# Kernel tuning notes

Hardware: AMD Instinct MI355X
Metric: run time of the kernel (lower is better)

Reference implementation:

```python
import jax, jax.numpy as jnp
import numpy as np

B, K, R, H = 64, 256, 4, 32


def setup_inputs() -> dict:
    key = jax.random.key(0)
    ks = jax.random.split(key, 24)
    rn = lambda k, s: jax.random.normal(k, s, dtype=jnp.float32)
    # F.normalize(dim=0) on per-sample [n, R] factors -> normalize columns (axis=1 batched)
    norm_cols = lambda x: x / jnp.linalg.norm(x, axis=1, keepdims=True)
    I = jnp.eye(K, dtype=jnp.float32)
    return dict(
        tensor_input=rn(ks[0], (B, 6, K, K)),
        seed_ic=rn(ks[1], (B, K)),
        seed_sir=rn(ks[2], (B, K)),
        seed_ic_conv=rn(ks[3], (B, K)),
        seed_sir_conv=rn(ks[4], (B, K)),
        scalars=rn(ks[5], (B, 2)),
        second_eig_interlink_out=rn(ks[6], (B,)),
        second_eig_interlink_in=rn(ks[7], (B,)),
        S1=I + 0.1 * rn(ks[8], (K, K)),
        S2=I + 0.1 * rn(ks[9], (K, K)),
        S3=I + 0.1 * rn(ks[10], (K, K)),
        S4=I + 0.1 * rn(ks[11], (K, K)),
        # CP factors (fresh random per sample in torch; fixed here for determinism)
        cp_A=norm_cols(rn(ks[12], (B, 6, R))),
        cp_B=norm_cols(rn(ks[13], (B, K, R))),
        cp_C=norm_cols(rn(ks[14], (B, K, R))),
        cp_W1=0.1 * rn(ks[15], (R, H, 3)), cp_b1=jnp.zeros((R, H), jnp.float32),
        cp_w2=0.1 * rn(ks[16], (R, H)), cp_b2=jnp.zeros((R,), jnp.float32),
        seed_W1=0.1 * rn(ks[17], (4, H, K)), seed_b1=jnp.zeros((4, H), jnp.float32),
        seed_w2=0.1 * rn(ks[18], (4, H)), seed_b2=jnp.zeros((4,), jnp.float32),
        fin_W1=0.1 * rn(ks[19], (H, R + 6)), fin_b1=jnp.zeros((H,), jnp.float32),
        fin_w2=0.1 * rn(ks[20], (H,)), fin_b2=jnp.zeros((), jnp.float32),
    )


def reference(tensor_input, seed_ic, seed_sir, seed_ic_conv, seed_sir_conv, scalars,
              second_eig_interlink_out, second_eig_interlink_in,
              S1, S2, S3, S4, cp_A, cp_B, cp_C,
              cp_W1, cp_b1, cp_w2, cp_b2,
              seed_W1, seed_b1, seed_w2, seed_b2,
              fin_W1, fin_b1, fin_w2, fin_b2):
    Kd = S1.shape[0]
    I = jnp.eye(Kd, dtype=tensor_input.dtype)
    ic1, ic2, sir1, sir2 = tensor_input[:, 0], tensor_input[:, 1], tensor_input[:, 2], tensor_input[:, 3]
    Z1r, Z2r = tensor_input[:, 4], tensor_input[:, 5]

    # MatrixTransform chains == plain batched matmuls (custom backward = standard matmul vjp)
    Z1 = ((ic1 @ S1) @ Z1r @ S2) @ jnp.swapaxes(sir2, -1, -2)   # [B,K,K]
    Z2 = ((sir1 @ S3) @ Z2r @ S4) @ jnp.swapaxes(ic2, -1, -2)   # [B,K,K]

    def spec_loss(val, M):
        ev = jnp.linalg.eigvalsh(M)                 # ascending, lower-triangle (matches torch)
        eig_loss = jnp.mean(jnp.abs(val - ev[1:5])) # k = min(5, K) = 5
        diff = jnp.mean(jnp.abs(M - I))             # reg_loss and diff_from_identity are identical
        off_loss = -jnp.mean(jnp.abs(M - jnp.diag(jnp.diag(M))))
        loss = eig_loss + 0.1 * diff + 0.1 * diff + 0.1 * off_loss
        return jnp.where(val != 0.0, loss, jnp.zeros_like(loss))  # torch: `if value`

    spec_out = jax.vmap(spec_loss)(second_eig_interlink_out, Z1).mean()
    spec_in = jax.vmap(spec_loss)(second_eig_interlink_in, Z2).mean()

    # S-matrix regularizers (batch-independent) + per-sample transform loss.
    # The torch list interleaves them, so the mean = 0.5*s_total + 0.5*mean(transform).
    sreg = lambda S: -jnp.mean(jnp.abs(S - I)) - jnp.mean(jnp.abs(S - jnp.diag(jnp.diag(S))))
    s_total = sreg(S1) + sreg(S2) + sreg(S3) + sreg(S4)
    transform = jnp.mean(jnp.abs(Z1 - Z1r), axis=(1, 2)) + jnp.mean(jnp.abs(Z2 - Z2r), axis=(1, 2))
    s_matrix_mean = 0.5 * s_total + 0.5 * transform.mean()

    # CP reconstruction loss on tensor with slots 4,5 replaced by Z1,Z2
    T_upd = jnp.concatenate([tensor_input[:, :4], Z1[:, None], Z2[:, None]], axis=1)  # [B,6,K,K]
    recon = jnp.einsum('bir,bjr,bkr->bijk', cp_A, cp_B, cp_C)
    cp_loss = jnp.mean((recon - T_upd) ** 2)

    # Per-rank tiny MLPs on factor means
    triple = jnp.stack([cp_A.mean(axis=1), cp_B.mean(axis=1), cp_C.mean(axis=1)], axis=-1)  # [B,R,3]
    h = jax.nn.relu(jnp.einsum('brd,rhd->brh', triple, cp_W1) + cp_b1[None])
    cp_s = jnp.einsum('brh,rh->br', h, cp_w2) + cp_b2[None]                                 # [B,R]

    seeds = jnp.stack([seed_ic, seed_sir, seed_ic_conv, seed_sir_conv], axis=1)             # [B,4,K]
    h2 = jax.nn.relu(jnp.einsum('bjk,jhk->bjh', seeds, seed_W1) + seed_b1[None])
    seed_s = jnp.einsum('bjh,jh->bj', h2, seed_w2) + seed_b2[None]                          # [B,4]

    combined = jnp.concatenate([cp_s, seed_s, scalars], axis=1)                             # [B,R+6]
    logits = jax.nn.relu(combined @ fin_W1.T + fin_b1) @ fin_w2 + fin_b2                    # [B]

    return (logits, spec_out, spec_in, cp_loss, s_matrix_mean)
```

## Files before the change

kernel.cpp:

```cpp
#include <hip/hip_runtime.h>
#include <hip/hip_fp16.h>

#define LM 24

#define OFF_MP    0ull
#define OFF_Q0    16777216ull
#define OFF_Q1    33554432ull
#define OFF_ZB    33554432ull
#define OFF_EIG   50331648ull
#define OFF_DIFFP (OFF_EIG + 4096ull)
#define OFF_OFFP  (OFF_DIFFP + 1024ull)
#define OFF_TRP   (OFF_OFFP + 1024ull)
#define OFF_SMALL (OFF_TRP + 1024ull)

typedef unsigned short ushort_t;
typedef short bf16x8 __attribute__((ext_vector_type(8)));
typedef float f32x4 __attribute__((ext_vector_type(4)));

static __device__ __forceinline__ ushort_t f2bf(float f) {
  unsigned u = __float_as_uint(f);
  unsigned r = (u + 0x7fffu + ((u >> 16) & 1u)) >> 16;
  return (ushort_t)r;
}
static __device__ __forceinline__ unsigned packbf(float a, float b) {
  return (unsigned)f2bf(a) | ((unsigned)f2bf(b) << 16);
}
static __device__ __forceinline__ float bflo(unsigned u) { return __uint_as_float(u << 16); }
static __device__ __forceinline__ float bfhi(unsigned u) { return __uint_as_float(u & 0xffff0000u); }
static __device__ __forceinline__ float b2f(ushort_t u) { return __uint_as_float(((unsigned)u) << 16); }
static __device__ __forceinline__ __half2 u2h2(unsigned u) { __half2 r; *reinterpret_cast<unsigned*>(&r) = u; return r; }
static __device__ __forceinline__ unsigned packh2(float a, float b) {
  return (unsigned)__half_as_ushort(__float2half_rn(a)) |
         ((unsigned)__half_as_ushort(__float2half_rn(b)) << 16);
}

template<bool ABF, int BMODE, bool INITP, bool REDUCE>
__global__ __launch_bounds__(256) void gemm_mfma(
    const void* __restrict__ A0, const void* __restrict__ A1, size_t sA,
    const void* __restrict__ B0, const void* __restrict__ B1, size_t sB,
    void* __restrict__ Cbase, size_t sC,
    const float* __restrict__ Zr0, const float* __restrict__ Zr1, size_t sZr,
    double* __restrict__ smallp, double* __restrict__ diffP,
    double* __restrict__ offP, double* __restrict__ trP)
{
  __shared__ ushort_t At[128][40];
  __shared__ ushort_t Bt[128][40];
  __shared__ float redsh[4][3];
  const int t = threadIdx.x;
  if (INITP && blockIdx.x == 0 && blockIdx.y == 0 && blockIdx.z == 0) {
    if (t < 2) smallp[t] = 0.0;
    if (t < 128) { diffP[t] = 0.0; offP[t] = 0.0; trP[t] = 0.0; }
  }
  const int b = blockIdx.z;
  const int bl = (b < 64) ? b : b - 64;
  const void* Ab_ = (b < 64) ? A0 : A1;
  const void* Bb_ = (b < 64) ? B0 : B1;
  const int tm = blockIdx.y * 128, tn = blockIdx.x * 128;
  const int w = t >> 6, l = t & 63;
  const int wr = w >> 1, wc = w & 1;
  const int fr = l & 15, kc = l >> 4;

  f32x4 acc[4][4] = {};

  for (int s8 = 0; s8 < 8; ++s8) {
    const int k0 = s8 << 5;
    #pragma unroll
    for (int cc = 0; cc < 2; ++cc) {
      int c = t + cc * 256;
      int row = c >> 2, q = c & 3;
      if (ABF) {
        const ushort_t* Ap = (const ushort_t*)Ab_ + (size_t)bl * sA + (size_t)(tm + row) * 256 + k0 + q * 8;
        *(uint4*)&At[row][q * 8] = *(const uint4*)Ap;
      } else {
        const float* Ap = (const float*)Ab_ + (size_t)bl * sA + (size_t)(tm + row) * 256 + k0 + q * 8;
        float4 f0 = *(const float4*)Ap, f1 = *(const float4*)(Ap + 4);
        uint4 u;
        u.x = packbf(f0.x, f0.y); u.y = packbf(f0.z, f0.w);
        u.z = packbf(f1.x, f1.y); u.w = packbf(f1.z, f1.w);
        *(uint4*)&At[row][q * 8] = u;
      }
    }
    if (BMODE == 1) {
      #pragma unroll
      for (int cc = 0; cc < 2; ++cc) {
        int c = t + cc * 256;
        int row = c >> 2, q = c & 3;
        const float* Bp = (const float*)Bb_ + (size_t)bl * sB + (size_t)(tn + row) * 256 + k0 + q * 8;
        float4 f0 = *(const float4*)Bp, f1 = *(const float4*)(Bp + 4);
        uint4 u;
        u.x = packbf(f0.x, f0.y); u.y = packbf(f0.z, f0.w);
        u.z = packbf(f1.x, f1.y); u.w = packbf(f1.z, f1.w);
        *(uint4*)&Bt[row][q * 8] = u;
      }
    } else {
      int k2 = t & 15, c = t >> 4;
      const float* Bp0 = (const float*)Bb_ + (size_t)bl * sB + (size_t)(k0 + 2 * k2) * 256 + tn + c * 8;
      const float* Bp1 = Bp0 + 256;
      float4 a0 = *(const float4*)Bp0, a1 = *(const float4*)(Bp0 + 4);
      float4 c0v = *(const float4*)Bp1, c1v = *(const float4*)(Bp1 + 4);
      float lo[8] = {a0.x,a0.y,a0.z,a0.w,a1.x,a1.y,a1.z,a1.w};
      float hi[8] = {c0v.x,c0v.y,c0v.z,c0v.w,c1v.x,c1v.y,c1v.z,c1v.w};
      unsigned* Bd = (unsigned*)&Bt[0][0];
      #pragma unroll
      for (int i = 0; i < 8; ++i) {
        int n = c * 8 + i;
        Bd[n * 20 + k2] = packbf(lo[i], hi[i]);
      }
    }
    __syncthreads();
    bf16x8 af[4], bfv[4];
    #pragma unroll
    for (int i = 0; i < 4; ++i) af[i] = *(const bf16x8*)&At[wr * 64 + i * 16 + fr][kc * 8];
    #pragma unroll
    for (int jj = 0; jj < 4; ++jj) bfv[jj] = *(const bf16x8*)&Bt[wc * 64 + jj * 16 + fr][kc * 8];
    #pragma unroll
    for (int i = 0; i < 4; ++i) {
      #pragma unroll
      for (int jj = 0; jj < 4; ++jj) {
        acc[i][jj] = __builtin_amdgcn_mfma_f32_16x16x32_bf16(af[i], bfv[jj], acc[i][jj], 0, 0, 0);
      }
    }
    __syncthreads();
  }

  ushort_t* Cp = (ushort_t*)Cbase + (size_t)b * sC;
  #pragma unroll
  for (int i = 0; i < 4; ++i) {
    #pragma unroll
    for (int q = 0; q < 4; ++q) {
      size_t rbase = (size_t)(tm + wr * 64 + i * 16 + kc * 4 + q) * 256;
      #pragma unroll
      for (int jj = 0; jj < 4; ++jj) {
        Cp[rbase + tn + wc * 64 + jj * 16 + fr] = f2bf(acc[i][jj][q]);
      }
    }
  }

  if (REDUCE) {
    const float* Zr_ = ((b < 64) ? Zr0 : Zr1) + (size_t)bl * sZr;
    float pd = 0.f, po = 0.f, ptr = 0.f;
    #pragma unroll
    for (int i = 0; i < 4; ++i) {
      #pragma unroll
      for (int q = 0; q < 4; ++q) {
        int row = tm + wr * 64 + i * 16 + kc * 4 + q;
        const float* ZrRow = Zr_ + (size_t)row * 256 + tn + wc * 64;
        #pragma unroll
        for (int jj = 0; jj < 4; ++jj) {
          int col = tn + wc * 64 + jj * 16 + fr;
          float c = acc[i][jj][q];
          float zr = ZrRow[jj * 16 + fr];
          bool diag = (row == col);
          pd += fabsf(c - (diag ? 1.0f : 0.0f));
          po += diag ? 0.0f : fabsf(c);
          ptr += fabsf(c - zr);
        }
      }
    }
    #pragma unroll
    for (int off = 32; off > 0; off >>= 1) {
      pd += __shfl_down(pd, off);
      po += __shfl_down(po, off);
      ptr += __shfl_down(ptr, off);
    }
    if (l == 0) { redsh[w][0] = pd; redsh[w][1] = po; redsh[w][2] = ptr; }
    __syncthreads();
    if (t == 0) {
      atomicAdd(&diffP[b], (double)(redsh[0][0] + redsh[1][0] + redsh[2][0] + redsh[3][0]));
      atomicAdd(&offP[b],  (double)(redsh[0][1] + redsh[1][1] + redsh[2][1] + redsh[3][1]));
      atomicAdd(&trP[b],   (double)(redsh[0][2] + redsh[1][2] + redsh[2][2] + redsh[3][2]));
    }
  }
}

__global__ __launch_bounds__(256) void symm_t(const ushort_t* __restrict__ Zb,
                                              unsigned* __restrict__ Mp)
{
  __shared__ unsigned Au[64][38];
  __shared__ unsigned Bu[64][38];
  const int blk = blockIdx.x;
  const int mtx = blk / 10, p = blk - mtx * 10;
  const int bi_t[10] = {0,0,0,0,1,1,1,2,2,3};
  const int bj_t[10] = {0,1,2,3,1,2,3,2,3,3};
  const int bi = bi_t[p], bj = bj_t[p];
  const ushort_t* Z = Zb + (size_t)mtx * 65536;
  const int t = threadIdx.x;
  #pragma unroll
  for (int it = 0; it < 4; ++it) {
    int idx = t + it * 256;
    int row = idx >> 4, jj = idx & 15;
    uint2 va = *(const uint2*)(Z + (size_t)(bi * 64 + row) * 256 + bj * 64 + jj * 4);
    uint2 vb = *(const uint2*)(Z + (size_t)(bj * 64 + row) * 256 + bi * 64 + jj * 4);
    Au[row][jj * 2] = va.x; Au[row][jj * 2 + 1] = va.y;
    Bu[row][jj * 2] = vb.x; Bu[row][jj * 2 + 1] = vb.y;
  }
  __syncthreads();
  const float SC = 0.5f * 0.015625f;
  const int r = t & 63, kbase = (t >> 6) * 8;
  unsigned* MpM = Mp + (size_t)mtx * 32768;
  const bool odd = (r & 1);
  #pragma unroll
  for (int i = 0; i < 8; ++i) {
    int k = kbase + i;
    unsigned a = Au[r][k];
    unsigned bu0 = Bu[2 * k][r >> 1], bu1 = Bu[2 * k + 1][r >> 1];
    float b0 = odd ? bfhi(bu0) : bflo(bu0);
    float b1 = odd ? bfhi(bu1) : bflo(bu1);
    MpM[(size_t)(bj * 32 + k) * 256 + bi * 64 + r] =
        packh2((bflo(a) + b0) * SC, (bfhi(a) + b1) * SC);
  }
  if (bi != bj) {
    #pragma unroll
    for (int i = 0; i < 8; ++i) {
      int k = kbase + i;
      unsigned a = Bu[r][k];
      unsigned au0 = Au[2 * k][r >> 1], au1 = Au[2 * k + 1][r >> 1];
      float a0 = odd ? bfhi(au0) : bflo(au0);
      float a1 = odd ? bfhi(au1) : bflo(au1);
      MpM[(size_t)(bi * 32 + k) * 256 + bj * 64 + r] =
          packh2((bflo(a) + a0) * SC, (bfhi(a) + a1) * SC);
    }
  }
}

struct LanSh {
  unsigned vpack[128];
  float wtmp[4][256];
  float red2[4][2];
  float red1[16];
  float alpha[LM];
  float betaArr[LM + 1];
  float beta2arr[LM + 1];
};
struct CpSh { float Bsh[4][256][4]; float Csh[4][256][4]; double red[4][256]; };
struct SregSh { double red[4][256]; };
struct HeadSh {
  float Wl[32][258];
  float seedsl[8][256];
  float hbuf2[8][128];
  float tri[8][4][3];
  float cps[8][4];
  float seds[8][4];
};
union MegaSh { LanSh lan; CpSh cp; SregSh sreg; HeadSh head; };

__global__ __launch_bounds__(1024, 1) void mega_kernel(
    const unsigned* __restrict__ Mp, float* __restrict__ eig,
    const float* __restrict__ ti, const ushort_t* __restrict__ Zb,
    const float* __restrict__ cpA, const float* __restrict__ cpB, const float* __restrict__ cpC,
    double* __restrict__ smallp,
    const float* __restrict__ S1, const float* __restrict__ S2,
    const float* __restrict__ S3, const float* __restrict__ S4,
    const float* __restrict__ seed_ic, const float* __restrict__ seed_sir,
    const float* __restrict__ seed_icc, const float* __restrict__ seed_sirc,
    const float* __restrict__ scalars,
    const float* __restrict__ cpW1, const float* __restrict__ cpb1,
    const float* __restrict__ cpw2, const float* __restrict__ cpb2,
    const float* __restrict__ sW1, const float* __restrict__ sb1,
    const float* __restrict__ sw2, const float* __restrict__ sb2,
    const float* __restrict__ fW1, const float* __restrict__ fb1,
    const float* __restrict__ fw2, const float* __restrict__ fb2,
    float* __restrict__ out)
{
  __shared__ MegaSh sh;
  const int bid = blockIdx.x;
  const int t = threadIdx.x;

  if (bid < 128) {
    int lane = t & 63, w16 = t >> 6;
    int r = t & 255, h = t >> 8;
    int mtx = bid;
    const unsigned* Mb = Mp + (size_t)mtx * 32768 + r;
    unsigned m[32];
    #pragma unroll
    for (int q = 0; q < 32; ++q) m[q] = Mb[(size_t)(h * 32 + q) * 256];

    unsigned u0 = (unsigned)r * 1103515245u + 12345u;
    float r0v = 0.05f + (float)((u0 >> 9) & 0x7FFF) * (1.0f / 32768.0f);
    float vt = 0.0f, vprev = 0.0f;
    {
      float nv = r0v * r0v;
      #pragma unroll
      for (int off = 32; off > 0; off >>= 1) nv += __shfl_down(nv, off);
      if (lane == 0) sh.lan.red1[w16] = nv;
    }
    __syncthreads();
    {
      float nrm2 = sh.lan.red1[0] + sh.lan.red1[1] + sh.lan.red1[2] + sh.lan.red1[3];
      vt = r0v * rsqrtf(nrm2);
      if (h == 0) {
        float vo = __shfl_down(vt, 1);
        if ((lane & 1) == 0) sh.lan.vpack[t >> 1] = packh2(vt, vo);
      }
    }
    __syncthreads();

    const uint4* vp4 = (const uint4*)sh.lan.vpack;
    float2* red2 = (float2*)&sh.lan.red2[0][0];
    float beta_prev = 0.0f;
    int meff = LM;
    for (int j = 0; j < LM; ++j) {
      __half2 h0v = u2h2(0u), h1v = u2h2(0u), h2v = u2h2(0u), h3v = u2h2(0u);
      #pragma unroll
      for (int q = 0; q < 8; ++q) {
        uint4 vu = vp4[h * 8 + q];
        h0v = __hfma2(u2h2(m[4 * q + 0]), u2h2(vu.x), h0v);
        h1v = __hfma2(u2h2(m[4 * q + 1]), u2h2(vu.y), h1v);
        h2v = __hfma2(u2h2(m[4 * q + 2]), u2h2(vu.z), h2v);
        h3v = __hfma2(u2h2(m[4 * q + 3]), u2h2(vu.w), h3v);
      }
      float2 f0 = __half22float2(h0v), f1 = __half22float2(h1v);
      float2 f2 = __half22float2(h2v), f3 = __half22float2(h3v);
      sh.lan.wtmp[h][r] = ((f0.x + f0.y) + (f1.x + f1.y)) + ((f2.x + f2.y) + (f3.x + f3.y));
      float wt = 0.0f;
      __syncthreads();
      if (h == 0) {
        wt = sh.lan.wtmp[0][r] + sh.lan.wtmp[1][r] + sh.lan.wtmp[2][r] + sh.lan.wtmp[3][r];
        float s1 = wt * vt, s3 = wt * wt;
        #pragma unroll
        for (int off = 32; off > 0; off >>= 1) {
          s1 += __shfl_down(s1, off);
          s3 += __shfl_down(s3, off);
        }
        if (lane == 0) red2[w16] = make_float2(s1, s3);
      }
      __syncthreads();
      float2 p0 = red2[0], p1 = red2[1], p2 = red2[2], p3 = red2[3];
      float S1v = ((p0.x + p1.x) + (p2.x + p3.x));
      float S3v = ((p0.y + p1.y) + (p2.y + p3.y));
      float bn2 = S3v - S1v * S1v - beta_prev * beta_prev;
      float bn = sqrtf(fmaxf(bn2, 1e-30f));
      if (t == 0) { sh.lan.alpha[j] = S1v; sh.lan.betaArr[j + 1] = bn; sh.lan.beta2arr[j + 1] = bn * bn; }
      if (bn < 1e-6f * (fabsf(S1v) + 1.0f)) { meff = j + 1; break; }
      if (h == 0) {
        float wn = (wt - S1v * vt - beta_prev * vprev) / bn;
        vprev = vt; vt = wn;
        float vo = __shfl_down(vt, 1);
        if ((lane & 1) == 0) sh.lan.vpack[t >> 1] = packh2(vt, vo);
      }
      beta_prev = bn;
      __syncthreads();
    }
    __syncthreads();

    if (w16 < 4) {
      float lo = 1e30f, hi = -1e30f;
      for (int i = 0; i < meff; ++i) {
        float bl = (i > 0) ? sh.lan.betaArr[i] : 0.0f;
        float bu = (i + 1 < meff) ? sh.lan.betaArr[i + 1] : 0.0f;
        lo = fminf(lo, sh.lan.alpha[i] - bl - bu);
        hi = fmaxf(hi, sh.lan.alpha[i] + bl + bu);
      }
      int q = w16 + 1; if (q > meff - 1) q = meff - 1;
      #pragma unroll
      for (int rr = 0; rr < 3; ++rr) {
        float step = (hi - lo) * (1.0f / 65.0f);
        float mid = lo + step * (float)(lane + 1);
        int cnt = 0;
        float d = sh.lan.alpha[0] - mid;
        if (fabsf(d) < 1e-20f) d = -1e-20f;
        cnt += (d < 0.0f);
        for (int i = 1; i < meff; ++i) {
          d = sh.lan.alpha[i] - mid - sh.lan.beta2arr[i] / d;
          if (fabsf(d) < 1e-20f) d = -1e-20f;
          cnt += (d < 0.0f);
        }
        unsigned long long mask = __ballot(cnt >= q + 1);
        if (mask == 0ULL) {
          lo = lo + step * 64.0f;
        } else {
          int idx = __ffsll(mask) - 1;
          float nlo = lo + step * (float)idx;
          hi = lo + step * (float)(idx + 1);
          lo = nlo;
        }
      }
      if (lane == 0) eig[mtx * 4 + w16] = 32.0f * (lo + hi);
    }
  } else if (bid < 224) {
    int g = t >> 8, tid = t & 255;
    int unit = (bid - 128) * 4 + g;
    int b = unit / 6, i = unit - b * 6;
    float (*Bsh)[4] = sh.cp.Bsh[g];
    float (*Csh)[4] = sh.cp.Csh[g];
    double* red = sh.cp.red[g];
    *(float4*)&Bsh[tid][0] = *(const float4*)(cpB + ((size_t)b * 256 + tid) * 4);
    *(float4*)&Csh[tid][0] = *(const float4*)(cpC + ((size_t)b * 256 + tid) * 4);
    float a0 = cpA[((size_t)b * 6 + i) * 4 + 0];
    float a1 = cpA[((size_t)b * 6 + i) * 4 + 1];
    float a2 = cpA[((size_t)b * 6 + i) * 4 + 2];
    float a3 = cpA[((size_t)b * 6 + i) * 4 + 3];
    __syncthreads();
    float c0 = Csh[tid][0], c1 = Csh[tid][1], c2 = Csh[tid][2], c3 = Csh[tid][3];
    double acc0 = 0, acc1 = 0;
    if (i < 4) {
      const float* T = ti + ((size_t)b * 6 + i) * 65536;
      #pragma unroll 4
      for (int j = 0; j < 256; j += 2) {
        float4 bj0 = *(const float4*)&Bsh[j][0];
        float4 bj1 = *(const float4*)&Bsh[j + 1][0];
        float r0 = a0 * bj0.x * c0 + a1 * bj0.y * c1 + a2 * bj0.z * c2 + a3 * bj0.w * c3;
        float r1 = a0 * bj1.x * c0 + a1 * bj1.y * c1 + a2 * bj1.z * c2 + a3 * bj1.w * c3;
        float d0 = r0 - T[(size_t)j * 256 + tid];
        float d1 = r1 - T[(size_t)(j + 1) * 256 + tid];
        acc0 += (double)d0 * (double)d0;
        acc1 += (double)d1 * (double)d1;
      }
    } else {
      const ushort_t* T = Zb + (size_t)((i == 4) ? b : 64 + b) * 65536;
      #pragma unroll 4
      for (int j = 0; j < 256; j += 2) {
        float4 bj0 = *(const float4*)&Bsh[j][0];
        float4 bj1 = *(const float4*)&Bsh[j + 1][0];
        float r0 = a0 * bj0.x * c0 + a1 * bj0.y * c1 + a2 * bj0.z * c2 + a3 * bj0.w * c3;
        float r1 = a0 * bj1.x * c0 + a1 * bj1.y * c1 + a2 * bj1.z * c2 + a3 * bj1.w * c3;
        float d0 = r0 - b2f(T[(size_t)j * 256 + tid]);
        float d1 = r1 - b2f(T[(size_t)(j + 1) * 256 + tid]);
        acc0 += (double)d0 * (double)d0;
        acc1 += (double)d1 * (double)d1;
      }
    }
    red[tid] = acc0 + acc1; __syncthreads();
    #pragma unroll
    for (int s = 128; s > 0; s >>= 1) { if (tid < s) red[tid] += red[tid + s]; __syncthreads(); }
    if (tid == 0) atomicAdd(&smallp[0], red[0]);
  } else if (bid < 228) {
    int g = t >> 8, tid = t & 255;
    int slot = (bid - 224) * 4 + g;
    int mnum = slot >> 2, quarter = slot & 3;
    const float* S = (mnum == 0) ? S1 : (mnum == 1) ? S2 : (mnum == 2) ? S3 : S4;
    double* red = sh.sreg.red[g];
    double tot = 0;
    int base = quarter * 16384;
    #pragma unroll 4
    for (int e = base + tid; e < base + 16384; e += 256) {
      int i = e >> 8, j = e & 255;
      float a = S[e];
      tot += (double)fabsf(a - (i == j ? 1.0f : 0.0f));
      if (i != j) tot += (double)fabsf(a);
    }
    red[tid] = tot; __syncthreads();
    #pragma unroll
    for (int s = 128; s > 0; s >>= 1) { if (tid < s) red[tid] += red[tid + s]; __syncthreads(); }
    if (tid == 0) atomicAdd(&smallp[1], -red[0] / 65536.0);
  } else {
    HeadSh& H = sh.head;
    const int b0 = (bid - 228) * 8;
    const int g = t >> 6, l = t & 63;
    const bool act = g < 8;
    const int b = b0 + (act ? g : 0);
    if (act) {
      if (l < 4) {
        float s = 0;
        #pragma unroll
        for (int i = 0; i < 6; ++i) s += cpA[((size_t)b * 6 + i) * 4 + l];
        H.tri[g][l][0] = s * (1.0f / 6.0f);
      }
      float4 sB = make_float4(0,0,0,0), sC = make_float4(0,0,0,0);
      for (int j = l; j < 256; j += 64) {
        float4 v = *(const float4*)(cpB + ((size_t)b * 256 + j) * 4);
        sB.x += v.x; sB.y += v.y; sB.z += v.z; sB.w += v.w;
        float4 w = *(const float4*)(cpC + ((size_t)b * 256 + j) * 4);
        sC.x += w.x; sC.y += w.y; sC.z += w.z; sC.w += w.w;
      }
      #pragma unroll
      for (int off = 32; off > 0; off >>= 1) {
        sB.x += __shfl_down(sB.x, off); sB.y += __shfl_down(sB.y, off);
        sB.z += __shfl_down(sB.z, off); sB.w += __shfl_down(sB.w, off);
        sC.x += __shfl_down(sC.x, off); sC.y += __shfl_down(sC.y, off);
        sC.z += __shfl_down(sC.z, off); sC.w += __shfl_down(sC.w, off);
      }
      if (l == 0) {
        H.tri[g][0][1] = sB.x * (1.0f/256.0f); H.tri[g][1][1] = sB.y * (1.0f/256.0f);
        H.tri[g][2][1] = sB.z * (1.0f/256.0f); H.tri[g][3][1] = sB.w * (1.0f/256.0f);
        H.tri[g][0][2] = sC.x * (1.0f/256.0f); H.tri[g][1][2] = sC.y * (1.0f/256.0f);
        H.tri[g][2][2] = sC.z * (1.0f/256.0f); H.tri[g][3][2] = sC.w * (1.0f/256.0f);
      }
      if (l < 4) {
        float s = 0;
        for (int hh = 0; hh < 32; ++hh) {
          float z = cpb1[l * 32 + hh];
          #pragma unroll
          for (int d = 0; d < 3; ++d) z += H.tri[g][l][d] * cpW1[(l * 32 + hh) * 3 + d];
          z = fmaxf(z, 0.0f);
          s += z * cpw2[l * 32 + hh];
        }
        H.cps[g][l] = s + cpb2[l];
      }
    }
    #pragma unroll 1
    for (int j = 0; j < 4; ++j) {
      __syncthreads();
      for (int idx = t; idx < 8192; idx += 1024) {
        H.Wl[idx >> 8][idx & 255] = sW1[(size_t)(j * 32 + (idx >> 8)) * 256 + (idx & 255)];
      }
      const float* sarr = (j == 0) ? seed_ic : (j == 1) ? seed_sir : (j == 2) ? seed_icc : seed_sirc;
      for (int idx = t; idx < 2048; idx += 1024) {
        H.seedsl[idx >> 8][idx & 255] = sarr[(size_t)(b0 + (idx >> 8)) * 256 + (idx & 255)];
      }
      __syncthreads();
      int bb = t >> 7, o = (t >> 2) & 31, kq = t & 3;
      float d = 0.f;
      #pragma unroll
      for (int kk = 0; kk < 64; kk += 4) {
        float4 w = *(const float4*)&H.Wl[o][kq * 64 + kk];
        float4 s = *(const float4*)&H.seedsl[bb][kq * 64 + kk];
        d += w.x * s.x + w.y * s.y + w.z * s.z + w.w * s.w;
      }
      d += __shfl_xor(d, 1);
      d += __shfl_xor(d, 2);
      if (kq == 0) {
        float z = fmaxf(d + sb1[j * 32 + o], 0.0f);
        H.hbuf2[bb][j * 32 + o] = z * sw2[j * 32 + o];
      }
    }
    __syncthreads();
    if (act && l < 4) {
      float s = 0;
      #pragma unroll
      for (int hh = 0; hh < 32; ++hh) s += H.hbuf2[g][l * 32 + hh];
      H.seds[g][l] = s + sb2[l];
    }
    __syncthreads();
    float av2 = 0.0f;
    if (act && l < 32) {
      float z = fb1[l];
      #pragma unroll
      for (int d = 0; d < 10; ++d) {
        float cd = (d < 4) ? H.cps[g][d] : (d < 8) ? H.seds[g][d - 4] : scalars[b * 2 + (d - 8)];
        z += cd * fW1[l * 10 + d];
      }
      z = fmaxf(z, 0.0f);
      av2 = z * fw2[l];
    }
    #pragma unroll
    for (int off = 16; off > 0; off >>= 1) av2 += __shfl_down(av2, off);
    if (act && l == 0) out[b] = av2 + fb2[0];
  }
}

__global__ __launch_bounds__(64) void combine_kernel(const float* __restrict__ eig,
    const double* __restrict__ diffP, const double* __restrict__ offP, const double* __restrict__ trP,
    const float* __restrict__ valo, const float* __restrict__ vali,
    const double* __restrict__ smallp, float* __restrict__ out)
{
  int l = threadIdx.x;
  float vo = valo[l], vi = vali[l];
  float el = 0, el2 = 0;
  #pragma unroll
  for (int e = 0; e < 4; ++e) {
    el  += fabsf(vo - eig[l * 4 + e]);
    el2 += fabsf(vi - eig[(64 + l) * 4 + e]);
  }
  float lo_ = el * 0.25f + 0.2f * (float)(diffP[l] * (1.0/65536.0)) - 0.1f * (float)(offP[l] * (1.0/65536.0));
  float li_ = el2 * 0.25f + 0.2f * (float)(diffP[64 + l] * (1.0/65536.0)) - 0.1f * (float)(offP[64 + l] * (1.0/65536.0));
  if (vo == 0.0f) lo_ = 0.0f;
  if (vi == 0.0f) li_ = 0.0f;
  float trb = (float)((trP[l] + trP[64 + l]) * (1.0/65536.0));
  #pragma unroll
  for (int off = 32; off > 0; off >>= 1) {
    lo_ += __shfl_down(lo_, off);
    li_ += __shfl_down(li_, off);
    trb += __shfl_down(trb, off);
  }
  if (l == 0) {
    out[64] = lo_ * (1.0f / 64.0f);
    out[65] = li_ * (1.0f / 64.0f);
    out[66] = (float)(smallp[0] / (64.0 * 6.0 * 65536.0));
    out[67] = 0.5f * (float)smallp[1] + 0.5f * (trb * (1.0f / 64.0f));
  }
}

extern "C" void kernel_launch(void* const* d_in, const int* in_sizes, int n_in,
                              void* d_out, int out_size, void* d_ws, size_t ws_size,
                              hipStream_t stream) {
  (void)in_sizes; (void)n_in; (void)out_size; (void)ws_size;
  const float* ti       = (const float*)d_in[0];
  const float* seed_ic  = (const float*)d_in[1];
  const float* seed_sir = (const float*)d_in[2];
  const float* seed_icc = (const float*)d_in[3];
  const float* seed_sirc= (const float*)d_in[4];
  const float* scalars  = (const float*)d_in[5];
  const float* valo     = (const float*)d_in[6];
  const float* vali     = (const float*)d_in[7];
  const float* S1p      = (const float*)d_in[8];
  const float* S2p      = (const float*)d_in[9];
  const float* S3p      = (const float*)d_in[10];
  const float* S4p      = (const float*)d_in[11];
  const float* cpA      = (const float*)d_in[12];
  const float* cpB      = (const float*)d_in[13];
  const float* cpC      = (const float*)d_in[14];
  const float* cpW1     = (const float*)d_in[15];
  const float* cpb1     = (const float*)d_in[16];
  const float* cpw2     = (const float*)d_in[17];
  const float* cpb2     = (const float*)d_in[18];
  const float* sW1      = (const float*)d_in[19];
  const float* sb1      = (const float*)d_in[20];
  const float* sw2      = (const float*)d_in[21];
  const float* sb2      = (const float*)d_in[22];
  const float* fW1      = (const float*)d_in[23];
  const float* fb1      = (const float*)d_in[24];
  const float* fw2      = (const float*)d_in[25];
  const float* fb2      = (const float*)d_in[26];

  char* ws = (char*)d_ws;
  unsigned* Mp     = (unsigned*)(ws + OFF_MP);
  ushort_t* Q0     = (ushort_t*)(ws + OFF_Q0);
  ushort_t* Q1     = (ushort_t*)(ws + OFF_Q1);
  ushort_t* Zb     = (ushort_t*)(ws + OFF_ZB);
  float*    eig    = (float*)(ws + OFF_EIG);
  double*   diffP  = (double*)(ws + OFF_DIFFP);
  double*   offP   = (double*)(ws + OFF_OFFP);
  double*   trP    = (double*)(ws + OFF_TRP);
  double*   smallp = (double*)(ws + OFF_SMALL);
  float*    out    = (float*)d_out;

  dim3 gg(2, 2, 128), gb(256);
  const size_t S6 = 6ull * 65536ull, S1b = 65536ull;
  gemm_mfma<false, 2, true, false><<<gg, gb, 0, stream>>>(
      (const void*)(ti + 0 * 65536), (const void*)(ti + 2 * 65536), S6,
      (const void*)S1p, (const void*)S3p, 0,
      (void*)Q0, S1b, nullptr, nullptr, 0, smallp, diffP, offP, trP);
  gemm_mfma<true, 2, false, false><<<gg, gb, 0, stream>>>(
      (const void*)Q0, (const void*)(Q0 + 64 * 65536), S1b,
      (const void*)(ti + 4 * 65536), (const void*)(ti + 5 * 65536), S6,
      (void*)Q1, S1b, nullptr, nullptr, 0, smallp, diffP, offP, trP);
  gemm_mfma<true, 2, false, false><<<gg, gb, 0, stream>>>(
      (const void*)Q1, (const void*)(Q1 + 64 * 65536), S1b,
      (const void*)S2p, (const void*)S4p, 0,
      (void*)Q0, S1b, nullptr, nullptr, 0, smallp, diffP, offP, trP);
  gemm_mfma<true, 1, false, true><<<gg, gb, 0, stream>>>(
      (const void*)Q0, (const void*)(Q0 + 64 * 65536), S1b,
      (const void*)(ti + 3 * 65536), (const void*)(ti + 1 * 65536), S6,
      (void*)Zb, S1b,
      ti + 4 * 65536, ti + 5 * 65536, S6, smallp, diffP, offP, trP);

  symm_t<<<1280, 256, 0, stream>>>(Zb, Mp);

  mega_kernel<<<236, 1024, 0, stream>>>(
      Mp, eig, ti, Zb, cpA, cpB, cpC, smallp,
      S1p, S2p, S3p, S4p,
      seed_ic, seed_sir, seed_icc, seed_sirc, scalars,
      cpW1, cpb1, cpw2, cpb2, sW1, sb1, sw2, sb2,
      fW1, fb1, fw2, fb2, out);

  combine_kernel<<<1, 64, 0, stream>>>(eig, diffP, offP, trP, valo, vali, smallp, out);
}
```

Before: 137.4 us.

## Fuse four chained batched GEMMs into one kernel keeping row band in LDS

Replaces four separate batched GEMM launches, which passed bf16 intermediates through global memory, with a single kernel. Each block owns a 128-row band of one matrix, keeps that band in LDS across all four multiplications, and register-prefetches the next B k-slice while the current one is consumed. This removes the intermediate global writes and reads and three launches. In exchange each launch has only 256 blocks of large LDS tiles with one block per CU, so the B operands are reread per band and occupancy is lower. Zeroing of the accumulators moves into a small separate init kernel.

```diff
diff --git a/kernel.cpp b/kernel.cpp
--- a/kernel.cpp
+++ b/kernel.cpp
@@ -4,8 +4,6 @@
 #define LM 24
 
 #define OFF_MP    0ull
-#define OFF_Q0    16777216ull
-#define OFF_Q1    33554432ull
 #define OFF_ZB    33554432ull
 #define OFF_EIG   50331648ull
 #define OFF_DIFFP (OFF_EIG + 4096ull)
@@ -34,141 +32,172 @@
          ((unsigned)__half_as_ushort(__float2half_rn(b)) << 16);
 }
 
-template<bool ABF, int BMODE, bool INITP, bool REDUCE>
-__global__ __launch_bounds__(256) void gemm_mfma(
-    const void* __restrict__ A0, const void* __restrict__ A1, size_t sA,
-    const void* __restrict__ B0, const void* __restrict__ B1, size_t sB,
-    void* __restrict__ Cbase, size_t sC,
-    const float* __restrict__ Zr0, const float* __restrict__ Zr1, size_t sZr,
-    double* __restrict__ smallp, double* __restrict__ diffP,
-    double* __restrict__ offP, double* __restrict__ trP)
+__global__ __launch_bounds__(128) void initk(double* smallp, double* diffP, double* offP, double* trP) {
+  int t = threadIdx.x;
+  if (t < 2) smallp[t] = 0.0;
+  diffP[t] = 0.0; offP[t] = 0.0; trP[t] = 0.0;
+}
+
+__global__ __launch_bounds__(256, 1) void chain_mfma(
+    const float* __restrict__ ti,
+    const float* __restrict__ S1p, const float* __restrict__ S2p,
+    const float* __restrict__ S3p, const float* __restrict__ S4p,
+    ushort_t* __restrict__ Zb,
+    double* __restrict__ diffP, double* __restrict__ offP, double* __restrict__ trP)
 {
-  __shared__ ushort_t At[128][40];
-  __shared__ ushort_t Bt[128][40];
+  __shared__ ushort_t Ab[128][264];
+  __shared__ ushort_t Bt[256][40];
   __shared__ float redsh[4][3];
   const int t = threadIdx.x;
-  if (INITP && blockIdx.x == 0 && blockIdx.y == 0 && blockIdx.z == 0) {
-    if (t < 2) smallp[t] = 0.0;
-    if (t < 128) { diffP[t] = 0.0; offP[t] = 0.0; trP[t] = 0.0; }
-  }
-  const int b = blockIdx.z;
-  const int bl = (b < 64) ? b : b - 64;
-  const void* Ab_ = (b < 64) ? A0 : A1;
-  const void* Bb_ = (b < 64) ? B0 : B1;
-  const int tm = blockIdx.y * 128, tn = blockIdx.x * 128;
+  const int bid = blockIdx.x;
+  const int b = bid & 127, band = bid >> 7;
+  const int ch = (b >= 64) ? 1 : 0;
+  const int bl = b & 63;
+  const float* A0 = ti + ((size_t)bl * 6 + (ch ? 2 : 0)) * 65536;
+  const float* Zr = ti + ((size_t)bl * 6 + (ch ? 5 : 4)) * 65536;
+  const float* Bn = ti + ((size_t)bl * 6 + (ch ? 1 : 3)) * 65536;
+  const float* Sa = ch ? S3p : S1p;
+  const float* Sb = ch ? S4p : S2p;
   const int w = t >> 6, l = t & 63;
-  const int wr = w >> 1, wc = w & 1;
   const int fr = l & 15, kc = l >> 4;
-
-  f32x4 acc[4][4] = {};
-
-  for (int s8 = 0; s8 < 8; ++s8) {
-    const int k0 = s8 << 5;
+  const int rb = band * 128;
+  const int pT = t >> 4, cT = t & 15;
+  unsigned* Bd = (unsigned*)&Bt[0][0];
+
+  #pragma unroll
+  for (int it = 0; it < 8; ++it) {
+    int idx = t + it * 256;
+    int row = idx >> 4, cg = (idx & 15) << 4;
+    const float* p = A0 + (size_t)(rb + row) * 256 + cg;
+    float4 f0 = *(const float4*)p, f1 = *(const float4*)(p + 4);
+    float4 f2v = *(const float4*)(p + 8), f3v = *(const float4*)(p + 12);
+    unsigned* dst = (unsigned*)&Ab[row][cg];
+    dst[0] = packbf(f0.x, f0.y); dst[1] = packbf(f0.z, f0.w);
+    dst[2] = packbf(f1.x, f1.y); dst[3] = packbf(f1.z, f1.w);
+    dst[4] = packbf(f2v.x, f2v.y); dst[5] = packbf(f2v.z, f2v.w);
+    dst[6] = packbf(f3v.x, f3v.y); dst[7] = packbf(f3v.z, f3v.w);
+  }
+
+  f32x4 acc[2][16];
+  for (int s = 0; s < 4; ++s) {
+    const float* Bp = (s == 0) ? Sa : (s == 1) ? Zr : (s == 2) ? Sb : Bn;
+    const bool modeT = (s < 3);
     #pragma unroll
-    for (int cc = 0; cc < 2; ++cc) {
-      int c = t + cc * 256;
-      int row = c >> 2, q = c & 3;
-      if (ABF) {
-        const ushort_t* Ap = (const ushort_t*)Ab_ + (size_t)bl * sA + (size_t)(tm + row) * 256 + k0 + q * 8;
-        *(uint4*)&At[row][q * 8] = *(const uint4*)Ap;
+    for (int i = 0; i < 2; ++i)
+      #pragma unroll
+      for (int jj = 0; jj < 16; ++jj) acc[i][jj] = (f32x4){0.f,0.f,0.f,0.f};
+
+    float4 rg0, rg1, rg2, rg3, rg4, rg5, rg6, rg7;
+    {
+      if (modeT) {
+        const float* r0p = Bp + (size_t)(2 * pT) * 256 + cT * 16;
+        const float* r1p = r0p + 256;
+        rg0 = *(const float4*)r0p;       rg1 = *(const float4*)(r0p + 4);
+        rg2 = *(const float4*)(r0p + 8); rg3 = *(const float4*)(r0p + 12);
+        rg4 = *(const float4*)r1p;       rg5 = *(const float4*)(r1p + 4);
+        rg6 = *(const float4*)(r1p + 8); rg7 = *(const float4*)(r1p + 12);
       } else {
-        const float* Ap = (const float*)Ab_ + (size_t)bl * sA + (size_t)(tm + row) * 256 + k0 + q * 8;
-        float4 f0 = *(const float4*)Ap, f1 = *(const float4*)(Ap + 4);
-        uint4 u;
-        u.x = packbf(f0.x, f0.y); u.y = packbf(f0.z, f0.w);
-        u.z = packbf(f1.x, f1.y); u.w = packbf(f1.z, f1.w);
-        *(uint4*)&At[row][q * 8] = u;
-      }
-    }
-    if (BMODE == 1) {
-      #pragma unroll
-      for (int cc = 0; cc < 2; ++cc) {
-        int c = t + cc * 256;
-        int row = c >> 2, q = c & 3;
-        const float* Bp = (const float*)Bb_ + (size_t)bl * sB + (size_t)(tn + row) * 256 + k0 + q * 8;
-        float4 f0 = *(const float4*)Bp, f1 = *(const float4*)(Bp + 4);
-        uint4 u;
-        u.x = packbf(f0.x, f0.y); u.y = packbf(f0.z, f0.w);
-        u.z = packbf(f1.x, f1.y); u.w = packbf(f1.z, f1.w);
-        *(uint4*)&Bt[row][q * 8] = u;
+        #define LDN(ii, dst) { int f = t + ii * 256; int n = f >> 3, fq = f & 7; \
+          dst = *(const float4*)(Bp + (size_t)n * 256 + fq * 4); }
+        LDN(0, rg0) LDN(1, rg1) LDN(2, rg2) LDN(3, rg3)
+        LDN(4, rg4) LDN(5, rg5) LDN(6, rg6) LDN(7, rg7)
+        #undef LDN
+      }
+    }
+
+    for (int ks = 0; ks < 8; ++ks) {
+      __syncthreads();
+      if (modeT) {
+        float lo[16] = {rg0.x,rg0.y,rg0.z,rg0.w, rg1.x,rg1.y,rg1.z,rg1.w,
+                        rg2.x,rg2.y,rg2.z,rg2.w, rg3.x,rg3.y,rg3.z,rg3.w};
+        float hi[16] = {rg4.x,rg4.y,rg4.z,rg4.w, rg5.x,rg5.y,rg5.z,rg5.w,
+                        rg6.x,rg6.y,rg6.z,rg6.w, rg7.x,rg7.y,rg7.z,rg7.w};
+        #pragma unroll
+        for (int i = 0; i < 16; ++i)
+          Bd[(cT * 16 + i) * 20 + pT] = packbf(lo[i], hi[i]);
+      } else {
+        #define STN(ii, src) { int f = t + ii * 256; int n = f >> 3, fq = f & 7; \
+          Bd[n * 20 + fq * 2] = packbf(src.x, src.y); Bd[n * 20 + fq * 2 + 1] = packbf(src.z, src.w); }
+        STN(0, rg0) STN(1, rg1) STN(2, rg2) STN(3, rg3)
+        STN(4, rg4) STN(5, rg5) STN(6, rg6) STN(7, rg7)
+        #undef STN
+      }
+      if (ks < 7) {
+        const int kn = (ks + 1) * 32;
+        if (modeT) {
+          const float* r0p = Bp + (size_t)(kn + 2 * pT) * 256 + cT * 16;
+          const float* r1p = r0p + 256;
+          rg0 = *(const float4*)r0p;       rg1 = *(const float4*)(r0p + 4);
+          rg2 = *(const float4*)(r0p + 8); rg3 = *(const float4*)(r0p + 12);
+          rg4 = *(const float4*)r1p;       rg5 = *(const float4*)(r1p + 4);
+          rg6 = *(const float4*)(r1p + 8); rg7 = *(const float4*)(r1p + 12);
+        } else {
+          #define LDN(ii, dst) { int f = t + ii * 256; int n = f >> 3, fq = f & 7; \
+            dst = *(const float4*)(Bp + (size_t)n * 256 + kn + fq * 4); }
+          LDN(0, rg0) LDN(1, rg1) LDN(2, rg2) LDN(3, rg3)
+          LDN(4, rg4) LDN(5, rg5) LDN(6, rg6) LDN(7, rg7)
+          #undef LDN
+        }
+      }
+      __syncthreads();
+      const int k0 = ks * 32;
+      bf16x8 af0 = *(const bf16x8*)&Ab[w * 32 + fr][k0 + kc * 8];
+      bf16x8 af1 = *(const bf16x8*)&Ab[w * 32 + 16 + fr][k0 + kc * 8];
+      #pragma unroll
+      for (int jj = 0; jj < 16; ++jj) {
+        bf16x8 bv = *(const bf16x8*)&Bt[jj * 16 + fr][kc * 8];
+        acc[0][jj] = __builtin_amdgcn_mfma_f32_16x16x32_bf16(af0, bv, acc[0][jj], 0, 0, 0);
+        acc[1][jj] = __builtin_amdgcn_mfma_f32_16x16x32_bf16(af1, bv, acc[1][jj], 0, 0, 0);
+      }
+    }
+
+    if (s < 3) {
+      __syncthreads();
+      #pragma unroll
+      for (int i = 0; i < 2; ++i) {
+        #pragma unroll
+        for (int q = 0; q < 4; ++q) {
+          int row = w * 32 + i * 16 + kc * 4 + q;
+          #pragma unroll
+          for (int jj = 0; jj < 16; ++jj)
+            Ab[row][jj * 16 + fr] = f2bf(acc[i][jj][q]);
+        }
       }
     } else {
-      int k2 = t & 15, c = t >> 4;
-      const float* Bp0 = (const float*)Bb_ + (size_t)bl * sB + (size_t)(k0 + 2 * k2) * 256 + tn + c * 8;
-      const float* Bp1 = Bp0 + 256;
-      float4 a0 = *(const float4*)Bp0, a1 = *(const float4*)(Bp0 + 4);
-      float4 c0v = *(const float4*)Bp1, c1v = *(const float4*)(Bp1 + 4);
-      float lo[8] = {a0.x,a0.y,a0.z,a0.w,a1.x,a1.y,a1.z,a1.w};
-      float hi[8] = {c0v.x,c0v.y,c0v.z,c0v.w,c1v.x,c1v.y,c1v.z,c1v.w};
-      unsigned* Bd = (unsigned*)&Bt[0][0];
-      #pragma unroll
-      for (int i = 0; i < 8; ++i) {
-        int n = c * 8 + i;
-        Bd[n * 20 + k2] = packbf(lo[i], hi[i]);
-      }
-    }
-    __syncthreads();
-    bf16x8 af[4], bfv[4];
-    #pragma unroll
-    for (int i = 0; i < 4; ++i) af[i] = *(const bf16x8*)&At[wr * 64 + i * 16 + fr][kc * 8];
-    #pragma unroll
-    for (int jj = 0; jj < 4; ++jj) bfv[jj] = *(const bf16x8*)&Bt[wc * 64 + jj * 16 + fr][kc * 8];
-    #pragma unroll
-    for (int i = 0; i < 4; ++i) {
-      #pragma unroll
-      for (int jj = 0; jj < 4; ++jj) {
-        acc[i][jj] = __builtin_amdgcn_mfma_f32_16x16x32_bf16(af[i], bfv[jj], acc[i][jj], 0, 0, 0);
-      }
-    }
-    __syncthreads();
-  }
-
-  ushort_t* Cp = (ushort_t*)Cbase + (size_t)b * sC;
-  #pragma unroll
-  for (int i = 0; i < 4; ++i) {
-    #pragma unroll
-    for (int q = 0; q < 4; ++q) {
-      size_t rbase = (size_t)(tm + wr * 64 + i * 16 + kc * 4 + q) * 256;
-      #pragma unroll
-      for (int jj = 0; jj < 4; ++jj) {
-        Cp[rbase + tn + wc * 64 + jj * 16 + fr] = f2bf(acc[i][jj][q]);
-      }
-    }
-  }
-
-  if (REDUCE) {
-    const float* Zr_ = ((b < 64) ? Zr0 : Zr1) + (size_t)bl * sZr;
-    float pd = 0.f, po = 0.f, ptr = 0.f;
-    #pragma unroll
-    for (int i = 0; i < 4; ++i) {
-      #pragma unroll
-      for (int q = 0; q < 4; ++q) {
-        int row = tm + wr * 64 + i * 16 + kc * 4 + q;
-        const float* ZrRow = Zr_ + (size_t)row * 256 + tn + wc * 64;
+      ushort_t* Cp = Zb + (size_t)b * 65536;
+      float pd = 0.f, po = 0.f, ptr = 0.f;
+      #pragma unroll
+      for (int i = 0; i < 2; ++i) {
         #pragma unroll
-        for (int jj = 0; jj < 4; ++jj) {
-          int col = tn + wc * 64 + jj * 16 + fr;
-          float c = acc[i][jj][q];
-          float zr = ZrRow[jj * 16 + fr];
-          bool diag = (row == col);
-          pd += fabsf(c - (diag ? 1.0f : 0.0f));
-          po += diag ? 0.0f : fabsf(c);
-          ptr += fabsf(c - zr);
+        for (int q = 0; q < 4; ++q) {
+          int row = rb + w * 32 + i * 16 + kc * 4 + q;
+          const float* ZrRow = Zr + (size_t)row * 256;
+          #pragma unroll
+          for (int jj = 0; jj < 16; ++jj) {
+            int col = jj * 16 + fr;
+            float c = acc[i][jj][q];
+            Cp[(size_t)row * 256 + col] = f2bf(c);
+            float zr = ZrRow[col];
+            bool diag = (row == col);
+            pd += fabsf(c - (diag ? 1.0f : 0.0f));
+            po += diag ? 0.0f : fabsf(c);
+            ptr += fabsf(c - zr);
+          }
         }
       }
-    }
-    #pragma unroll
-    for (int off = 32; off > 0; off >>= 1) {
-      pd += __shfl_down(pd, off);
-      po += __shfl_down(po, off);
-      ptr += __shfl_down(ptr, off);
-    }
-    if (l == 0) { redsh[w][0] = pd; redsh[w][1] = po; redsh[w][2] = ptr; }
-    __syncthreads();
-    if (t == 0) {
-      atomicAdd(&diffP[b], (double)(redsh[0][0] + redsh[1][0] + redsh[2][0] + redsh[3][0]));
-      atomicAdd(&offP[b],  (double)(redsh[0][1] + redsh[1][1] + redsh[2][1] + redsh[3][1]));
-      atomicAdd(&trP[b],   (double)(redsh[0][2] + redsh[1][2] + redsh[2][2] + redsh[3][2]));
+      #pragma unroll
+      for (int off = 32; off > 0; off >>= 1) {
+        pd += __shfl_down(pd, off);
+        po += __shfl_down(po, off);
+        ptr += __shfl_down(ptr, off);
+      }
+      if (l == 0) { redsh[w][0] = pd; redsh[w][1] = po; redsh[w][2] = ptr; }
+      __syncthreads();
+      if (t == 0) {
+        atomicAdd(&diffP[b], (double)(redsh[0][0] + redsh[1][0] + redsh[2][0] + redsh[3][0]));
+        atomicAdd(&offP[b],  (double)(redsh[0][1] + redsh[1][1] + redsh[2][1] + redsh[3][1]));
+        atomicAdd(&trP[b],   (double)(redsh[0][2] + redsh[1][2] + redsh[2][2] + redsh[3][2]));
+      }
     }
   }
 }
@@ -605,8 +634,6 @@
 
   char* ws = (char*)d_ws;
   unsigned* Mp     = (unsigned*)(ws + OFF_MP);
-  ushort_t* Q0     = (ushort_t*)(ws + OFF_Q0);
-  ushort_t* Q1     = (ushort_t*)(ws + OFF_Q1);
   ushort_t* Zb     = (ushort_t*)(ws + OFF_ZB);
   float*    eig    = (float*)(ws + OFF_EIG);
   double*   diffP  = (double*)(ws + OFF_DIFFP);
@@ -615,25 +642,9 @@
   double*   smallp = (double*)(ws + OFF_SMALL);
   float*    out    = (float*)d_out;
 
-  dim3 gg(2, 2, 128), gb(256);
-  const size_t S6 = 6ull * 65536ull, S1b = 65536ull;
-  gemm_mfma<false, 2, true, false><<<gg, gb, 0, stream>>>(
-      (const void*)(ti + 0 * 65536), (const void*)(ti + 2 * 65536), S6,
-      (const void*)S1p, (const void*)S3p, 0,
-      (void*)Q0, S1b, nullptr, nullptr, 0, smallp, diffP, offP, trP);
-  gemm_mfma<true, 2, false, false><<<gg, gb, 0, stream>>>(
-      (const void*)Q0, (const void*)(Q0 + 64 * 65536), S1b,
-      (const void*)(ti + 4 * 65536), (const void*)(ti + 5 * 65536), S6,
-      (void*)Q1, S1b, nullptr, nullptr, 0, smallp, diffP, offP, trP);
-  gemm_mfma<true, 2, false, false><<<gg, gb, 0, stream>>>(
-      (const void*)Q1, (const void*)(Q1 + 64 * 65536), S1b,
-      (const void*)S2p, (const void*)S4p, 0,
-      (void*)Q0, S1b, nullptr, nullptr, 0, smallp, diffP, offP, trP);
-  gemm_mfma<true, 1, false, true><<<gg, gb, 0, stream>>>(
-      (const void*)Q0, (const void*)(Q0 + 64 * 65536), S1b,
-      (const void*)(ti + 3 * 65536), (const void*)(ti + 1 * 65536), S6,
-      (void*)Zb, S1b,
-      ti + 4 * 65536, ti + 5 * 65536, S6, smallp, diffP, offP, trP);
+  initk<<<1, 128, 0, stream>>>(smallp, diffP, offP, trP);
+
+  chain_mfma<<<256, 256, 0, stream>>>(ti, S1p, S2p, S3p, S4p, Zb, diffP, offP, trP);
 
   symm_t<<<1280, 256, 0, stream>>>(Zb, Mp);
 
```

New measurement: 187.6 us. +36.6%, slower.
